# Optimization experiments

Measured on AMD Instinct MI355X. Metric: run time of the kernel, lower is better.

## Reference

```python
import jax, jax.numpy as jnp
import numpy as np

G, N, F = 16, 2048, 32          # graphs, nodes/graph, node feature width
E = 32768                        # edges per graph (avg degree 16)
INPUT_DIM = N * F                # 65536, matches reshape in original forward
H, L = 512, 64                   # VAE hidden width, latent dim
BN_EPS = 1e-5
NEG_SLOPE = 0.01                 # nn.LeakyReLU default


def setup_inputs() -> dict:
    key = jax.random.key(0)
    ks = jax.random.split(key, 18)
    f32 = jnp.float32
    inp = {
        "x": jax.random.normal(ks[0], (G, N, F), dtype=f32),
        "edge_index": jax.random.randint(ks[1], (G, 2, E), 0, N, dtype=jnp.int32),
        "eps": jax.random.normal(ks[2], (G, L), dtype=f32),
        # GCNConv weight + bias
        "W_gcn": jax.random.normal(ks[3], (F, F), dtype=f32) / np.sqrt(F),
        "b_gcn": jnp.zeros((F,), dtype=f32),
        # BatchNorm1d(num_features) affine params
        "bn_gamma": jnp.ones((F,), dtype=f32),
        "bn_beta": jnp.zeros((F,), dtype=f32),
        # VAE encoder trunk + mean / log_var heads
        "W_enc": jax.random.normal(ks[4], (INPUT_DIM, H), dtype=f32) / np.sqrt(INPUT_DIM),
        "b_enc": jnp.zeros((H,), dtype=f32),
        "W_mu": jax.random.normal(ks[5], (H, L), dtype=f32) / np.sqrt(H),
        "b_mu": jnp.zeros((L,), dtype=f32),
        "W_lv": jax.random.normal(ks[6], (H, L), dtype=f32) / np.sqrt(H),
        "b_lv": jnp.zeros((L,), dtype=f32),
        # VAE decoder
        "W_dec1": jax.random.normal(ks[7], (L, H), dtype=f32) / np.sqrt(L),
        "b_dec1": jnp.zeros((H,), dtype=f32),
        "W_dec2": jax.random.normal(ks[8], (H, INPUT_DIM), dtype=f32) / np.sqrt(H),
        "b_dec2": jnp.zeros((INPUT_DIM,), dtype=f32),
    }
    return inp


def _gcn_conv(xg, eig, W_gcn, b_gcn):
    # PyG GCNConv: add self-loops, symmetric normalization D^-1/2 A D^-1/2
    src, dst = eig[0], eig[1]
    loop = jnp.arange(N, dtype=src.dtype)
    src = jnp.concatenate([src, loop])
    dst = jnp.concatenate([dst, loop])
    deg = jax.ops.segment_sum(jnp.ones(src.shape, dtype=xg.dtype), dst, num_segments=N)
    dinv = jax.lax.rsqrt(deg)  # deg >= 1 due to self-loops
    xw = xg @ W_gcn                                  # [N, F]
    coef = dinv[src] * dinv[dst]                     # [E+N]
    msg = xw[src] * coef[:, None]                    # gather + scale
    return jax.ops.segment_sum(msg, dst, num_segments=N) + b_gcn  # scatter-add


def reference(x, edge_index, eps, W_gcn, b_gcn, bn_gamma, bn_beta,
              W_enc, b_enc, W_mu, b_mu, W_lv, b_lv,
              W_dec1, b_dec1, W_dec2, b_dec2):
    # convolute(): per-graph GCN conv -> BatchNorm1d (batch stats over that graph's
    # nodes) -> tanh -> dropout (identity in eval) -> concat. Vectorized via vmap.
    h = jax.vmap(_gcn_conv, in_axes=(0, 0, None, None))(x, edge_index, W_gcn, b_gcn)  # [G,N,F]
    mu_n = h.mean(axis=1, keepdims=True)
    var_n = h.var(axis=1, keepdims=True)  # biased variance, as torch BN uses in normalization
    h = (h - mu_n) * jax.lax.rsqrt(var_n + BN_EPS) * bn_gamma + bn_beta
    h = jnp.tanh(h)
    xs = h.reshape(G, INPUT_DIM)
    # VariationalExample forward
    henc = jax.nn.leaky_relu(xs @ W_enc + b_enc, NEG_SLOPE)   # [G, H]
    mean = henc @ W_mu + b_mu                                  # [G, L]
    log_var = henc @ W_lv + b_lv                               # [G, L]
    z = mean + jnp.exp(0.5 * log_var) * eps                    # reparameterize
    hd = jax.nn.leaky_relu(z @ W_dec1 + b_dec1, NEG_SLOPE)     # [G, H]
    x_hat = hd @ W_dec2 + b_dec2                               # [G, INPUT_DIM]
    return x_hat, mean, log_var
```

## Files before the change

### kernel.cpp

```cpp
#include <hip/hip_runtime.h>
#include <hip/hip_bf16.h>

#define NG 16
#define NN 2048
#define NF 32
#define NE 32768
#define IND 65536
#define HD 512
#define LD 64

typedef unsigned int u32;


__global__ void k_xwdeg(const float* __restrict__ x, const float* __restrict__ Wg,
                        float* __restrict__ xw, const int* __restrict__ ei,
                        u32* __restrict__ deg){
  __shared__ float ws[32][33];
  __shared__ float xsh[8][32];
  int t = threadIdx.x;
  int bid = blockIdx.x;
  if (bid < 4096){
    for (int i = t; i < 1024; i += 256) ws[i >> 5][i & 31] = Wg[i];
    int base = bid * 8;
    int r = t >> 5, f = t & 31;
    xsh[r][f] = x[(base + r) * 32 + f];
    __syncthreads();
    float acc = 0.f;
    #pragma unroll
    for (int k = 0; k < 32; ++k) acc += xsh[r][k] * ws[k][f];
    xw[(base + r) * 32 + f] = acc;
  } else {
    int idx = (bid - 4096) * 256 + t;
    int g = idx >> 15, e = idx & (NE - 1);
    int dst = ei[(g * 2 + 1) * NE + e];
    atomicAdd(&deg[g * NN + dst], 1u);
  }
}

__global__ void k_prefix(const u32* __restrict__ deg, u32* __restrict__ offs,
                         float* __restrict__ dinv, u32* __restrict__ cursor){
  int g = blockIdx.x, t = threadIdx.x;
  const u32* dg = deg + g * NN;
  u32 loc[8]; u32 s = 0;
  #pragma unroll
  for (int i = 0; i < 8; ++i){ loc[i] = s; s += dg[t * 8 + i]; }
  __shared__ u32 bs[256];
  bs[t] = s; __syncthreads();
  for (int d = 1; d < 256; d <<= 1){
    u32 v = (t >= d) ? bs[t - d] : 0u;
    __syncthreads();
    bs[t] += v;
    __syncthreads();
  }
  u32 base = bs[t] - s;
  #pragma unroll
  for (int i = 0; i < 8; ++i){
    int n = t * 8 + i;
    offs[g * NN + n] = g * NE + base + loc[i];
    dinv[g * NN + n] = rsqrtf((float)(dg[n] + 1u));
    cursor[g * NN + n] = 0u;
  }
}

__global__ void k_sortedges(const int* __restrict__ ei, const u32* __restrict__ offs,
                            u32* __restrict__ cursor, u32* __restrict__ sorted){
  int idx = blockIdx.x * 256 + threadIdx.x;
  int g = idx >> 15, e = idx & (NE - 1);
  int src = ei[g * 2 * NE + e];
  int dst = ei[(g * 2 + 1) * NE + e];
  u32 pos = atomicAdd(&cursor[g * NN + dst], 1u);
  sorted[offs[g * NN + dst] + pos] = (u32)src;
}

__global__ void k_gather(const u32* __restrict__ sorted, const u32* __restrict__ offs,
                         const u32* __restrict__ deg, const float* __restrict__ dinv,
                         const float* __restrict__ xw, const float* __restrict__ bg,
                         float* __restrict__ h){
  int tid = blockIdx.x * 256 + threadIdx.x;
  int qp = tid & 3, n = (tid >> 2) & (NN - 1), g = tid >> 13;
  int gn = g * NN + n;
  u32 o0 = offs[gn];
  u32 cnt = deg[gn];
  float dn = dinv[gn];
  const float4* xw4 = (const float4*)xw;
  float4 a0 = make_float4(0.f,0.f,0.f,0.f), a1 = a0;
  for (u32 e = 0; e < cnt; ++e){
    u32 src = sorted[o0 + e];
    float c = dinv[g * NN + src] * dn;
    const float4* xr = xw4 + (size_t)(g * NN + src) * 8 + qp * 2;
    float4 v0 = xr[0], v1 = xr[1];
    a0.x += c*v0.x; a0.y += c*v0.y; a0.z += c*v0.z; a0.w += c*v0.w;
    a1.x += c*v1.x; a1.y += c*v1.y; a1.z += c*v1.z; a1.w += c*v1.w;
  }
  float c2 = dn * dn;
  const float4* xr = xw4 + (size_t)gn * 8 + qp * 2;
  float4 v0 = xr[0], v1 = xr[1];
  float4 b0 = ((const float4*)bg)[qp * 2], b1 = ((const float4*)bg)[qp * 2 + 1];
  a0.x += c2*v0.x + b0.x; a0.y += c2*v0.y + b0.y; a0.z += c2*v0.z + b0.z; a0.w += c2*v0.w + b0.w;
  a1.x += c2*v1.x + b1.x; a1.y += c2*v1.y + b1.y; a1.z += c2*v1.z + b1.z; a1.w += c2*v1.w + b1.w;
  float4* hp = (float4*)h + (size_t)gn * 8 + qp * 2;
  hp[0] = a0; hp[1] = a1;
}


__global__ void k_bnstat(const float* __restrict__ h, float* __restrict__ pstat){
  int g = blockIdx.x >> 3, s = blockIdx.x & 7;
  int t = threadIdx.x, f = t & 31, r = t >> 5;
  float s1 = 0.f, s2 = 0.f;
  for (int it = 0; it < 32; ++it){
    int n = s * 256 + it * 8 + r;
    float v = h[(size_t)(g * NN + n) * 32 + f];
    s1 += v; s2 += v * v;
  }
  __shared__ float l1[256], l2[256];
  l1[t] = s1; l2[t] = s2;
  __syncthreads();
  if (t < 32){
    float a = 0.f, b = 0.f;
    #pragma unroll
    for (int r2 = 0; r2 < 8; ++r2){ a += l1[r2 * 32 + t]; b += l2[r2 * 32 + t]; }
    pstat[((g * 8 + s) * 32 + t) * 2 + 0] = a;
    pstat[((g * 8 + s) * 32 + t) * 2 + 1] = b;
  }
}


__global__ __launch_bounds__(256) void k_gemvenc(const float* __restrict__ h,
    const float* __restrict__ pstat, const float* __restrict__ gamma,
    const float* __restrict__ beta, const float* __restrict__ B,
    float* __restrict__ part){
  __shared__ float ash[128 * 17];
  __shared__ float ssc[512], ssh[512];
  int t = threadIdx.x;
  int k0 = blockIdx.x * 128;
  for (int i = t; i < 512; i += 256){
    int g = i >> 5, f = i & 31;
    float s1 = 0.f, s2 = 0.f;
    #pragma unroll
    for (int s = 0; s < 8; ++s){
      s1 += pstat[((g * 8 + s) * 32 + f) * 2 + 0];
      s2 += pstat[((g * 8 + s) * 32 + f) * 2 + 1];
    }
    float mean = s1 * (1.f / NN);
    float var  = s2 * (1.f / NN) - mean * mean;
    float sc = gamma[f] * rsqrtf(var + 1e-5f);
    ssc[i] = sc;
    ssh[i] = beta[f] - mean * sc;
  }
  __syncthreads();
  for (int idx = t; idx < 2048; idx += 256){
    int i = idx & 127, g = idx >> 7;
    int f = i & 31;
    float v = h[(size_t)g * IND + k0 + i];
    ash[i * 17 + g] = tanhf(v * ssc[g * 32 + f] + ssh[g * 32 + f]);
  }
  __syncthreads();
  float acc[32];
  #pragma unroll
  for (int i = 0; i < 32; ++i) acc[i] = 0.f;
  const float2* bp = (const float2*)(B + (size_t)k0 * 512) + t;
  for (int kk = 0; kk < 128; kk += 8){
    float2 bv[8];
    #pragma unroll
    for (int u = 0; u < 8; ++u) bv[u] = bp[(size_t)(kk + u) * 256];
    #pragma unroll
    for (int u = 0; u < 8; ++u){
      const float* ap = &ash[(kk + u) * 17];
      #pragma unroll
      for (int m = 0; m < 16; ++m){
        acc[2*m]   += ap[m] * bv[u].x;
        acc[2*m+1] += ap[m] * bv[u].y;
      }
    }
  }
  float* pp = part + (size_t)blockIdx.x * 8192 + t * 2;
  #pragma unroll
  for (int m = 0; m < 16; ++m)
    *(float2*)(pp + (size_t)m * 512) = make_float2(acc[2*m], acc[2*m+1]);
}

__global__ void k_encred1(const float* __restrict__ part, float* __restrict__ p2){
  int idx = blockIdx.x * 256 + threadIdx.x;
  int out = idx & 8191, grp = idx >> 13;
  const float* p = part + (size_t)grp * 64 * 8192 + out;
  float s = 0.f;
  #pragma unroll 8
  for (int c = 0; c < 64; ++c) s += p[(size_t)c * 8192];
  p2[idx] = s;
}

__global__ void k_encred2(const float* __restrict__ p2, const float* __restrict__ be,
                          float* __restrict__ henc){
  int out = blockIdx.x * 256 + threadIdx.x;
  int n = out & 511;
  float s = be[n];
  #pragma unroll
  for (int g = 0; g < 8; ++g) s += p2[g * 8192 + out];
  henc[out] = s > 0.f ? s : 0.01f * s;
}

__global__ __launch_bounds__(512) void k_headdec(const float* __restrict__ henc,
    const float* __restrict__ Wmu, const float* __restrict__ bmu,
    const float* __restrict__ Wlv, const float* __restrict__ blv,
    const float* __restrict__ eps, const float* __restrict__ W1,
    const float* __restrict__ b1, float* __restrict__ hdT, float* __restrict__ outp){
  int g = blockIdx.x, t = threadIdx.x;
  __shared__ float hsh[512];
  __shared__ float zsh[64];
  hsh[t] = henc[g * 512 + t];
  __syncthreads();
  int l = t >> 3, r = t & 7;
  float am = 0.f, av = 0.f;
  for (int k = r; k < 512; k += 8){
    float hh = hsh[k];
    am += hh * Wmu[k * 64 + l];
    av += hh * Wlv[k * 64 + l];
  }
  #pragma unroll
  for (int d = 1; d < 8; d <<= 1){
    am += __shfl_xor(am, d);
    av += __shfl_xor(av, d);
  }
  if (r == 0){
    float mean = am + bmu[l];
    float lv   = av + blv[l];
    float z = mean + expf(0.5f * lv) * eps[g * 64 + l];
    zsh[l] = z;
    outp[1048576 + g * 64 + l] = mean;
    outp[1049600 + g * 64 + l] = lv;
  }
  __syncthreads();
  float a = 0.f;
  #pragma unroll
  for (int k = 0; k < 64; ++k) a += zsh[k] * W1[k * 512 + t];
  a += b1[t];
  a = a > 0.f ? a : 0.01f * a;
  hdT[t * 16 + g] = a;
}


__global__ __launch_bounds__(256) void k_gemvdec(const float* __restrict__ A,
                          const float* __restrict__ B,
                          float* __restrict__ part){
  __shared__ float ash[128 * 16];
  int t = threadIdx.x;
  int ks = blockIdx.x & 3;
  int nb = blockIdx.x >> 2;
  for (int i = t; i < 2048; i += 256) ash[i] = A[ks * 2048 + i];
  __syncthreads();
  float acc[32];
  #pragma unroll
  for (int i = 0; i < 32; ++i) acc[i] = 0.f;
  const float2* bp = (const float2*)(B + (size_t)ks * 128 * 65536) + nb * 256 + t;
  for (int kk = 0; kk < 128; kk += 8){
    float2 bv[8];
    #pragma unroll
    for (int u = 0; u < 8; ++u) bv[u] = bp[(size_t)(kk + u) * 32768];
    #pragma unroll
    for (int u = 0; u < 8; ++u){
      const float* ap = &ash[(kk + u) * 16];
      #pragma unroll
      for (int m = 0; m < 16; ++m){
        acc[2*m]   += ap[m] * bv[u].x;
        acc[2*m+1] += ap[m] * bv[u].y;
      }
    }
  }
  float* pp = part + (size_t)ks * 1048576 + nb * 512 + t * 2;
  #pragma unroll
  for (int m = 0; m < 16; ++m)
    *(float2*)(pp + (size_t)m * 65536) = make_float2(acc[2*m], acc[2*m+1]);
}

__global__ void k_decred(const float4* __restrict__ part, const float4* __restrict__ b2,
                         float4* __restrict__ outp){
  int idx = blockIdx.x * 256 + threadIdx.x;
  float4 s = b2[idx & 16383];
  #pragma unroll
  for (int ks = 0; ks < 4; ++ks){
    float4 p = part[(size_t)ks * 262144 + idx];
    s.x += p.x; s.y += p.y; s.z += p.z; s.w += p.w;
  }
  outp[idx] = s;
}


extern "C" void kernel_launch(void* const* d_in, const int* in_sizes, int n_in,
                              void* d_out, int out_size, void* d_ws, size_t ws_size,
                              hipStream_t stream){
  const float* x     = (const float*)d_in[0];
  const int*   ei    = (const int*)d_in[1];
  const float* eps   = (const float*)d_in[2];
  const float* Wg    = (const float*)d_in[3];
  const float* bg    = (const float*)d_in[4];
  const float* gamma = (const float*)d_in[5];
  const float* beta  = (const float*)d_in[6];
  const float* Wenc  = (const float*)d_in[7];
  const float* benc  = (const float*)d_in[8];
  const float* Wmu   = (const float*)d_in[9];
  const float* bmu   = (const float*)d_in[10];
  const float* Wlv   = (const float*)d_in[11];
  const float* blv   = (const float*)d_in[12];
  const float* Wd1   = (const float*)d_in[13];
  const float* bd1   = (const float*)d_in[14];
  const float* Wd2   = (const float*)d_in[15];
  const float* bd2   = (const float*)d_in[16];
  float* outp = (float*)d_out;

  char* ws = (char*)d_ws;
  const size_t OFF_XW     = 0;
  const size_t OFF_H      = 4194304;
  const size_t OFF_DEG    = 8388608;
  const size_t OFF_DINV   = 8519680;
  const size_t OFF_CURSOR = 8650752;
  const size_t OFF_PSTAT  = 8781824;
  const size_t OFF_HENC   = 8814592;
  const size_t OFF_HDT    = 8847360;
  const size_t OFF_P2     = 8880128;
  const size_t OFF_PART   = 9142272;
  const size_t OFF_SORT   = OFF_PART;
  const size_t OFF_OFFS   = OFF_PART + 2097152;

  float* xw     = (float*)(ws + OFF_XW);
  float* h      = (float*)(ws + OFF_H);
  u32*   deg    = (u32*)  (ws + OFF_DEG);
  float* dinv   = (float*)(ws + OFF_DINV);
  u32*   cursor = (u32*)  (ws + OFF_CURSOR);
  float* pstat  = (float*)(ws + OFF_PSTAT);
  float* henc   = (float*)(ws + OFF_HENC);
  float* hdT    = (float*)(ws + OFF_HDT);
  float* p2     = (float*)(ws + OFF_P2);
  float* part   = (float*)(ws + OFF_PART);
  u32*   sorted = (u32*)  (ws + OFF_SORT);
  u32*   offs   = (u32*)  (ws + OFF_OFFS);

  hipMemsetAsync(ws + OFF_DEG, 0, 131072, stream);

  k_xwdeg    <<<6144, 256, 0, stream>>>(x, Wg, xw, ei, deg);
  k_prefix   <<<16,   256, 0, stream>>>(deg, offs, dinv, cursor);
  k_sortedges<<<2048, 256, 0, stream>>>(ei, offs, cursor, sorted);
  k_gather   <<<512,  256, 0, stream>>>(sorted, offs, deg, dinv, xw, bg, h);
  k_bnstat   <<<128,  256, 0, stream>>>(h, pstat);

  k_gemvenc  <<<512, 256, 0, stream>>>(h, pstat, gamma, beta, Wenc, part);
  k_encred1  <<<256, 256, 0, stream>>>(part, p2);
  k_encred2  <<<32,  256, 0, stream>>>(p2, benc, henc);

  k_headdec  <<<16, 512, 0, stream>>>(henc, Wmu, bmu, Wlv, blv, eps, Wd1, bd1, hdT, outp);

  k_gemvdec  <<<512, 256, 0, stream>>>(hdT, Wd2, part);
  k_decred   <<<1024, 256, 0, stream>>>((const float4*)part, (const float4*)bd2, (float4*)outp);
}
```

Before: 181.4 us.

## Fuse BN stats into gather, encoder bias into head, and split-K reduction into decoder GEMV

The BatchNorm statistics pass is folded into the gather kernel using wavefront shuffles plus float atomics into a zeroed stats buffer. The encoder's second reduction and LeakyReLU move into the head kernel. The decoder GEMV now does its split-K reduction in shared memory and writes output with bias directly, which removes the partial buffer and the decode reduction kernel. Three launches and their intermediate global traffic go away, at the cost of atomic contention, nondeterministic summation order and larger shared memory in the decoder.

```diff
diff --git a/kernel.cpp b/kernel.cpp
--- a/kernel.cpp
+++ b/kernel.cpp
@@ -72,11 +72,12 @@
   sorted[offs[g * NN + dst] + pos] = (u32)src;
 }
 
-__global__ void k_gather(const u32* __restrict__ sorted, const u32* __restrict__ offs,
-                         const u32* __restrict__ deg, const float* __restrict__ dinv,
-                         const float* __restrict__ xw, const float* __restrict__ bg,
-                         float* __restrict__ h){
-  int tid = blockIdx.x * 256 + threadIdx.x;
+__global__ void k_gatherbn(const u32* __restrict__ sorted, const u32* __restrict__ offs,
+                           const u32* __restrict__ deg, const float* __restrict__ dinv,
+                           const float* __restrict__ xw, const float* __restrict__ bg,
+                           float* __restrict__ h, float* __restrict__ pstat){
+  int t = threadIdx.x;
+  int tid = blockIdx.x * 256 + t;
   int qp = tid & 3, n = (tid >> 2) & (NN - 1), g = tid >> 13;
   int gn = g * NN + n;
   u32 o0 = offs[gn];
@@ -100,27 +101,30 @@
   a1.x += c2*v1.x + b1.x; a1.y += c2*v1.y + b1.y; a1.z += c2*v1.z + b1.z; a1.w += c2*v1.w + b1.w;
   float4* hp = (float4*)h + (size_t)gn * 8 + qp * 2;
   hp[0] = a0; hp[1] = a1;
-}
-
-
-__global__ void k_bnstat(const float* __restrict__ h, float* __restrict__ pstat){
-  int g = blockIdx.x >> 3, s = blockIdx.x & 7;
-  int t = threadIdx.x, f = t & 31, r = t >> 5;
-  float s1 = 0.f, s2 = 0.f;
-  for (int it = 0; it < 32; ++it){
-    int n = s * 256 + it * 8 + r;
-    float v = h[(size_t)(g * NN + n) * 32 + f];
-    s1 += v; s2 += v * v;
-  }
-  __shared__ float l1[256], l2[256];
-  l1[t] = s1; l2[t] = s2;
-  __syncthreads();
-  if (t < 32){
-    float a = 0.f, b = 0.f;
-    #pragma unroll
-    for (int r2 = 0; r2 < 8; ++r2){ a += l1[r2 * 32 + t]; b += l2[r2 * 32 + t]; }
-    pstat[((g * 8 + s) * 32 + t) * 2 + 0] = a;
-    pstat[((g * 8 + s) * 32 + t) * 2 + 1] = b;
+  float s0x=a0.x, s0y=a0.y, s0z=a0.z, s0w=a0.w, s1x=a1.x, s1y=a1.y, s1z=a1.z, s1w=a1.w;
+  float q0x=a0.x*a0.x, q0y=a0.y*a0.y, q0z=a0.z*a0.z, q0w=a0.w*a0.w;
+  float q1x=a1.x*a1.x, q1y=a1.y*a1.y, q1z=a1.z*a1.z, q1w=a1.w*a1.w;
+  #pragma unroll
+  for (int d = 4; d < 64; d <<= 1){
+    s0x += __shfl_xor(s0x, d); s0y += __shfl_xor(s0y, d);
+    s0z += __shfl_xor(s0z, d); s0w += __shfl_xor(s0w, d);
+    s1x += __shfl_xor(s1x, d); s1y += __shfl_xor(s1y, d);
+    s1z += __shfl_xor(s1z, d); s1w += __shfl_xor(s1w, d);
+    q0x += __shfl_xor(q0x, d); q0y += __shfl_xor(q0y, d);
+    q0z += __shfl_xor(q0z, d); q0w += __shfl_xor(q0w, d);
+    q1x += __shfl_xor(q1x, d); q1y += __shfl_xor(q1y, d);
+    q1z += __shfl_xor(q1z, d); q1w += __shfl_xor(q1w, d);
+  }
+  if ((t & 63) < 4){
+    float* ps = pstat + (g * 32 + qp * 8) * 2;
+    atomicAdd(ps + 0,  s0x); atomicAdd(ps + 1,  q0x);
+    atomicAdd(ps + 2,  s0y); atomicAdd(ps + 3,  q0y);
+    atomicAdd(ps + 4,  s0z); atomicAdd(ps + 5,  q0z);
+    atomicAdd(ps + 6,  s0w); atomicAdd(ps + 7,  q0w);
+    atomicAdd(ps + 8,  s1x); atomicAdd(ps + 9,  q1x);
+    atomicAdd(ps + 10, s1y); atomicAdd(ps + 11, q1y);
+    atomicAdd(ps + 12, s1z); atomicAdd(ps + 13, q1z);
+    atomicAdd(ps + 14, s1w); atomicAdd(ps + 15, q1w);
   }
 }
 
@@ -134,15 +138,9 @@
   int t = threadIdx.x;
   int k0 = blockIdx.x * 128;
   for (int i = t; i < 512; i += 256){
-    int g = i >> 5, f = i & 31;
-    float s1 = 0.f, s2 = 0.f;
-    #pragma unroll
-    for (int s = 0; s < 8; ++s){
-      s1 += pstat[((g * 8 + s) * 32 + f) * 2 + 0];
-      s2 += pstat[((g * 8 + s) * 32 + f) * 2 + 1];
-    }
-    float mean = s1 * (1.f / NN);
-    float var  = s2 * (1.f / NN) - mean * mean;
+    int f = i & 31;
+    float mean = pstat[i * 2] * (1.f / NN);
+    float var  = pstat[i * 2 + 1] * (1.f / NN) - mean * mean;
     float sc = gamma[f] * rsqrtf(var + 1e-5f);
     ssc[i] = sc;
     ssh[i] = beta[f] - mean * sc;
@@ -189,17 +187,8 @@
   p2[idx] = s;
 }
 
-__global__ void k_encred2(const float* __restrict__ p2, const float* __restrict__ be,
-                          float* __restrict__ henc){
-  int out = blockIdx.x * 256 + threadIdx.x;
-  int n = out & 511;
-  float s = be[n];
-  #pragma unroll
-  for (int g = 0; g < 8; ++g) s += p2[g * 8192 + out];
-  henc[out] = s > 0.f ? s : 0.01f * s;
-}
-
-__global__ __launch_bounds__(512) void k_headdec(const float* __restrict__ henc,
+__global__ __launch_bounds__(512) void k_headdec(const float* __restrict__ p2,
+    const float* __restrict__ be,
     const float* __restrict__ Wmu, const float* __restrict__ bmu,
     const float* __restrict__ Wlv, const float* __restrict__ blv,
     const float* __restrict__ eps, const float* __restrict__ W1,
@@ -207,7 +196,11 @@
   int g = blockIdx.x, t = threadIdx.x;
   __shared__ float hsh[512];
   __shared__ float zsh[64];
-  hsh[t] = henc[g * 512 + t];
+  float hv = be[t];
+  #pragma unroll
+  for (int grp = 0; grp < 8; ++grp) hv += p2[grp * 8192 + g * 512 + t];
+  hv = hv > 0.f ? hv : 0.01f * hv;
+  hsh[t] = hv;
   __syncthreads();
   int l = t >> 3, r = t & 7;
   float am = 0.f, av = 0.f;
@@ -241,24 +234,26 @@
 
 __global__ __launch_bounds__(256) void k_gemvdec(const float* __restrict__ A,
                           const float* __restrict__ B,
-                          float* __restrict__ part){
-  __shared__ float ash[128 * 16];
+                          const float* __restrict__ bias,
+                          float* __restrict__ outp){
+  __shared__ float ash[8192];
   int t = threadIdx.x;
-  int ks = blockIdx.x & 3;
-  int nb = blockIdx.x >> 2;
-  for (int i = t; i < 2048; i += 256) ash[i] = A[ks * 2048 + i];
-  __syncthreads();
+  int nt = blockIdx.x;
+  for (int i = t; i < 8192; i += 256) ash[i] = A[i];
+  __syncthreads();
+  int cp = t & 63;
+  int kq = t >> 6;
   float acc[32];
   #pragma unroll
   for (int i = 0; i < 32; ++i) acc[i] = 0.f;
-  const float2* bp = (const float2*)(B + (size_t)ks * 128 * 65536) + nb * 256 + t;
+  const float2* bp = (const float2*)B + (size_t)(kq * 128) * 32768 + nt * 64 + cp;
   for (int kk = 0; kk < 128; kk += 8){
     float2 bv[8];
     #pragma unroll
     for (int u = 0; u < 8; ++u) bv[u] = bp[(size_t)(kk + u) * 32768];
     #pragma unroll
     for (int u = 0; u < 8; ++u){
-      const float* ap = &ash[(kk + u) * 16];
+      const float* ap = &ash[(kq * 128 + kk + u) * 16];
       #pragma unroll
       for (int m = 0; m < 16; ++m){
         acc[2*m]   += ap[m] * bv[u].x;
@@ -266,22 +261,27 @@
       }
     }
   }
-  float* pp = part + (size_t)ks * 1048576 + nb * 512 + t * 2;
-  #pragma unroll
-  for (int m = 0; m < 16; ++m)
-    *(float2*)(pp + (size_t)m * 65536) = make_float2(acc[2*m], acc[2*m+1]);
-}
-
-__global__ void k_decred(const float4* __restrict__ part, const float4* __restrict__ b2,
-                         float4* __restrict__ outp){
-  int idx = blockIdx.x * 256 + threadIdx.x;
-  float4 s = b2[idx & 16383];
-  #pragma unroll
-  for (int ks = 0; ks < 4; ++ks){
-    float4 p = part[(size_t)ks * 262144 + idx];
-    s.x += p.x; s.y += p.y; s.z += p.z; s.w += p.w;
-  }
-  outp[idx] = s;
+  __syncthreads();
+  #pragma unroll
+  for (int m = 0; m < 16; ++m){
+    ash[kq * 2048 + (m * 2 + 0) * 64 + cp] = acc[2*m];
+    ash[kq * 2048 + (m * 2 + 1) * 64 + cp] = acc[2*m+1];
+  }
+  __syncthreads();
+  #pragma unroll
+  for (int jj = 0; jj < 4; ++jj){
+    int idx = t * 4 + jj;
+    int m = idx >> 6, c = idx & 63;
+    float sx = 0.f, sy = 0.f;
+    #pragma unroll
+    for (int q = 0; q < 4; ++q){
+      sx += ash[q * 2048 + (m * 2 + 0) * 64 + c];
+      sy += ash[q * 2048 + (m * 2 + 1) * 64 + c];
+    }
+    float2 bb = ((const float2*)bias)[nt * 64 + c];
+    *(float2*)(outp + (size_t)m * 65536 + nt * 128 + c * 2) =
+        make_float2(sx + bb.x, sy + bb.y);
+  }
 }
 
 
@@ -311,43 +311,38 @@
   const size_t OFF_XW     = 0;
   const size_t OFF_H      = 4194304;
   const size_t OFF_DEG    = 8388608;
-  const size_t OFF_DINV   = 8519680;
-  const size_t OFF_CURSOR = 8650752;
-  const size_t OFF_PSTAT  = 8781824;
-  const size_t OFF_HENC   = 8814592;
-  const size_t OFF_HDT    = 8847360;
-  const size_t OFF_P2     = 8880128;
-  const size_t OFF_PART   = 9142272;
+  const size_t OFF_PSTAT  = 8519680;
+  const size_t OFF_DINV   = 8523776;
+  const size_t OFF_CURSOR = 8654848;
+  const size_t OFF_HDT    = 8785920;
+  const size_t OFF_P2     = 8818688;
+  const size_t OFF_PART   = 9109504;
   const size_t OFF_SORT   = OFF_PART;
   const size_t OFF_OFFS   = OFF_PART + 2097152;
 
   float* xw     = (float*)(ws + OFF_XW);
   float* h      = (float*)(ws + OFF_H);
   u32*   deg    = (u32*)  (ws + OFF_DEG);
+  float* pstat  = (float*)(ws + OFF_PSTAT);
   float* dinv   = (float*)(ws + OFF_DINV);
   u32*   cursor = (u32*)  (ws + OFF_CURSOR);
-  float* pstat  = (float*)(ws + OFF_PSTAT);
-  float* henc   = (float*)(ws + OFF_HENC);
   float* hdT    = (float*)(ws + OFF_HDT);
   float* p2     = (float*)(ws + OFF_P2);
   float* part   = (float*)(ws + OFF_PART);
   u32*   sorted = (u32*)  (ws + OFF_SORT);
   u32*   offs   = (u32*)  (ws + OFF_OFFS);
 
-  hipMemsetAsync(ws + OFF_DEG, 0, 131072, stream);
+  hipMemsetAsync(ws + OFF_DEG, 0, 135168, stream);
 
   k_xwdeg    <<<6144, 256, 0, stream>>>(x, Wg, xw, ei, deg);
   k_prefix   <<<16,   256, 0, stream>>>(deg, offs, dinv, cursor);
   k_sortedges<<<2048, 256, 0, stream>>>(ei, offs, cursor, sorted);
-  k_gather   <<<512,  256, 0, stream>>>(sorted, offs, deg, dinv, xw, bg, h);
-  k_bnstat   <<<128,  256, 0, stream>>>(h, pstat);
+  k_gatherbn <<<512,  256, 0, stream>>>(sorted, offs, deg, dinv, xw, bg, h, pstat);
 
   k_gemvenc  <<<512, 256, 0, stream>>>(h, pstat, gamma, beta, Wenc, part);
   k_encred1  <<<256, 256, 0, stream>>>(part, p2);
-  k_encred2  <<<32,  256, 0, stream>>>(p2, benc, henc);
-
-  k_headdec  <<<16, 512, 0, stream>>>(henc, Wmu, bmu, Wlv, blv, eps, Wd1, bd1, hdT, outp);
-
-  k_gemvdec  <<<512, 256, 0, stream>>>(hdT, Wd2, part);
-  k_decred   <<<1024, 256, 0, stream>>>((const float4*)part, (const float4*)bd2, (float4*)outp);
-}
+
+  k_headdec  <<<16, 512, 0, stream>>>(p2, benc, Wmu, bmu, Wlv, blv, eps, Wd1, bd1, hdT, outp);
+
+  k_gemvdec  <<<512, 256, 0, stream>>>(hdT, Wd2, bd2, outp);
+}
```

Result: slower. 224.7 us (+23.9%).
